# Optimization experiments

Measured on AMD Instinct MI355X. Metric: run time of the kernel, lower is better.

The kernel has to match this reference:

```python
import jax, jax.numpy as jnp
import numpy as np

LN_EPS = 1e-5
NEG_SLOPE = 0.2
INF = float((1 << 32) - 1)


def _ln(x, g, b):
    m = x.mean(-1, keepdims=True)
    v = ((x - m) ** 2).mean(-1, keepdims=True)
    return (x - m) * jax.lax.rsqrt(v + LN_EPS) * g + b


def setup_inputs() -> dict:
    B, M, NPG = 128, 256, 192      # graphs, max nodes per graph, actual nodes per graph
    N = B * NPG                    # 24576 total nodes
    E = N * 16                     # 393216 edges (avg degree 16)
    d, H, Od = 256, 4, 64          # input/attn dim, heads, per-head dim
    out_dim = 256
    key = jax.random.key(0)
    ks = jax.random.split(key, 24)
    s = 0.05
    p = lambda k, sh: jax.random.normal(k, sh, jnp.float32) * s

    node_feat = jax.random.normal(ks[0], (N, d), jnp.float32)
    edge_feat = jax.random.normal(ks[1], (E, d), jnp.float32)
    edge_index = jax.random.randint(ks[2], (2, E), 0, N)
    ptr = jnp.arange(B + 1, dtype=jnp.int32) * NPG
    row_valid = jnp.arange(M) < NPG
    attn_mask = jnp.broadcast_to(row_valid[None, :, None] & row_valid[None, None, :], (B, M, M))

    return dict(
        node_feat=node_feat, attn_mask=attn_mask, edge_feat=edge_feat,
        edge_index=edge_index, num_nodes=N, ptr=ptr,
        Wq=p(ks[3], (d, H * Od)), Wk=p(ks[4], (d, H * Od)), Wv=p(ks[5], (d, H * Od)),
        alphaQ=p(ks[6], (H, Od)), alphaK=p(ks[7], (H, Od)), attn_bias=p(ks[8], (H, Od)),
        gin_eps=jnp.zeros((), jnp.float32),
        gin_W1=p(ks[9], (d, 2 * d)), gin_b1=jnp.zeros((2 * d,), jnp.float32),
        gin_W2=p(ks[10], (2 * d, d)), gin_b2=jnp.zeros((d,), jnp.float32),
        ln1_g=jnp.ones((d,), jnp.float32), ln1_b=jnp.zeros((d,), jnp.float32),
        ln2_g=jnp.ones((d,), jnp.float32), ln2_b=jnp.zeros((d,), jnp.float32),
        ff_W1=p(ks[11], (2 * d, out_dim)), ff_b1=jnp.zeros((out_dim,), jnp.float32),
        ff_W2=p(ks[12], (out_dim, out_dim)), ff_b2=jnp.zeros((out_dim,), jnp.float32),
    )


def reference(node_feat, attn_mask, edge_feat, edge_index, num_nodes, ptr,
              Wq, Wk, Wv, alphaQ, alphaK, attn_bias,
              gin_eps, gin_W1, gin_b1, gin_W2, gin_b2,
              ln1_g, ln1_b, ln2_g, ln2_b,
              ff_W1, ff_b1, ff_W2, ff_b2):
    B, M = attn_mask.shape[:2]
    N, d = node_feat.shape
    H = alphaQ.shape[0]

    # graph -> dense batch layout (scatter by (graph, local position))
    node_ids = jnp.arange(N)
    batch_id = jnp.searchsorted(ptr, node_ids, side='right') - 1
    local = node_ids - ptr[batch_id]
    attn_input = jnp.zeros((B, M, d), node_feat.dtype).at[batch_id, local].set(node_feat)

    # GAT-style additive multi-head attention
    Qp = (attn_input @ Wq).reshape(B, M, H, -1)
    Kp = (attn_input @ Wk).reshape(B, M, H, -1)
    Vp = (attn_input @ Wv).reshape(B, M, H, -1)
    aQ = jnp.einsum('bmhd,hd->bmh', Qp, alphaQ)
    aK = jnp.einsum('bmhd,hd->bmh', Kp, alphaK)
    w = jax.nn.leaky_relu(aQ[:, :, None, :] + aK[:, None, :, :], NEG_SLOPE)  # [B,Q,K,H]
    w = jnp.where(attn_mask[..., None], w, -INF)
    w = jax.nn.softmax(w, axis=2)
    attn_out = (jnp.einsum('bqkh,bkhd->bqhd', w, Vp) + attn_bias).reshape(B, M, -1)

    attn_res = _ln(attn_out + attn_input, ln1_g, ln1_b)[batch_id, local]  # back to [N, d]

    # GIN conv: relu(x[dst] + e) scatter-summed to src, then 2-layer MLP
    msg = jax.nn.relu(node_feat[edge_index[1]] + edge_feat)
    agg = jax.ops.segment_sum(msg, edge_index[0], num_segments=num_nodes)
    h = (1.0 + gin_eps) * node_feat + agg
    gin = jax.nn.relu(h @ gin_W1 + gin_b1) @ gin_W2 + gin_b2
    gin_res = _ln(gin + node_feat, ln2_g, ln2_b)

    x = jnp.concatenate([gin_res, attn_res], axis=-1)  # [N, 2d]
    return jax.nn.relu(x @ ff_W1 + ff_b1) @ ff_W2 + ff_b2
```

## Files before the change

### kernel.cpp

```cpp
#include <hip/hip_runtime.h>

#define LN_EPS 1e-5f
#define NEG_SLOPE 0.2f

typedef __attribute__((ext_vector_type(8))) short short8;
typedef __attribute__((ext_vector_type(4))) float f32x4;

__device__ __forceinline__ unsigned short f2bf(float f) {
  union { float f; unsigned int u; } v;
  v.f = f;
  unsigned int r = v.u + 0x7fffu + ((v.u >> 16) & 1u);
  return (unsigned short)(r >> 16);
}
__device__ __forceinline__ float bf2f(unsigned short u) {
  union { unsigned int u; float f; } v;
  v.u = ((unsigned int)u) << 16;
  return v.f;
}

__global__ __launch_bounds__(256) void k_prep(
    const float* __restrict__ Wv, const float* __restrict__ gW1,
    const float* __restrict__ gW2, const float* __restrict__ fW1,
    const float* __restrict__ fW2, unsigned short* __restrict__ wvt,
    unsigned short* __restrict__ w1t, unsigned short* __restrict__ w2t,
    unsigned short* __restrict__ fw1t, unsigned short* __restrict__ fw2t,
    const float* __restrict__ Wq, const float* __restrict__ Wk,
    const float* __restrict__ alphaQ, const float* __restrict__ alphaK,
    float* __restrict__ wqa, float* __restrict__ wka) {
  if (blockIdx.x == 2048) {
    int t = threadIdx.x;
    for (int h = 0; h < 4; ++h) {
      float sq = 0.f, sk = 0.f;
      for (int od = 0; od < 64; ++od) {
        sq += Wq[t * 256 + h * 64 + od] * alphaQ[h * 64 + od];
        sk += Wk[t * 256 + h * 64 + od] * alphaK[h * 64 + od];
      }
      wqa[t * 4 + h] = sq;
      wka[t * 4 + h] = sk;
    }
    return;
  }
  int i = blockIdx.x * 256 + threadIdx.x;
  const float* src;
  unsigned short* dst;
  int K, N, base;
  if (i < 65536) {
    src = Wv; dst = wvt; K = 256; N = 256; base = 0;
  } else if (i < 196608) {
    src = gW1; dst = w1t; K = 256; N = 512; base = 65536;
  } else if (i < 327680) {
    src = gW2; dst = w2t; K = 512; N = 256; base = 196608;
  } else if (i < 458752) {
    src = fW1; dst = fw1t; K = 512; N = 256; base = 327680;
  } else {
    src = fW2; dst = fw2t; K = 256; N = 256; base = 458752;
  }
  int j = i - base;
  int n = j / K, k = j - n * K;
  dst[j] = f2bf(src[(size_t)k * N + n]);
}

__global__ __launch_bounds__(256) void k_cast(const float* __restrict__ in,
                                              unsigned short* __restrict__ out,
                                              int total4) {
  int i = blockIdx.x * 256 + threadIdx.x;
  if (i < total4) {
    float4 v = ((const float4*)in)[i];
    ushort4 o;
    o.x = f2bf(v.x);
    o.y = f2bf(v.y);
    o.z = f2bf(v.z);
    o.w = f2bf(v.w);
    ((ushort4*)out)[i] = o;
  }
}

__global__ __launch_bounds__(64) void k_aqk(
    const float* __restrict__ X, const float* __restrict__ wqa,
    const float* __restrict__ wka, float* __restrict__ aQ,
    float* __restrict__ aK) {
  int n = blockIdx.x;
  int lane = threadIdx.x;
  float4 x = *(const float4*)(X + (size_t)n * 256 + lane * 4);
  float sq[4], sk[4];
#pragma unroll
  for (int h = 0; h < 4; ++h) {
    int d0 = lane * 4;
    sq[h] = x.x * wqa[(d0 + 0) * 4 + h] + x.y * wqa[(d0 + 1) * 4 + h] +
            x.z * wqa[(d0 + 2) * 4 + h] + x.w * wqa[(d0 + 3) * 4 + h];
    sk[h] = x.x * wka[(d0 + 0) * 4 + h] + x.y * wka[(d0 + 1) * 4 + h] +
            x.z * wka[(d0 + 2) * 4 + h] + x.w * wka[(d0 + 3) * 4 + h];
  }
#pragma unroll
  for (int off = 32; off; off >>= 1) {
#pragma unroll
    for (int h = 0; h < 4; ++h) {
      sq[h] += __shfl_xor(sq[h], off);
      sk[h] += __shfl_xor(sk[h], off);
    }
  }
  if (lane == 0) {
#pragma unroll
    for (int h = 0; h < 4; ++h) {
      aQ[(size_t)n * 4 + h] = sq[h];
      aK[(size_t)n * 4 + h] = sk[h];
    }
  }
}

template <bool RELU, bool BIAS, bool OUTBF>
__global__ __launch_bounds__(256) void k_gemm16(
    const unsigned short* __restrict__ A, const unsigned short* __restrict__ Bt,
    const float* __restrict__ bias, void* __restrict__ Cv, int M, int N,
    int K) {
  __shared__ uint4 As[1024];
  __shared__ uint4 Bs[1024];
  const int tid = threadIdx.x;
  const int wid = tid >> 6;
  const int lane = tid & 63;
  const int row0 = blockIdx.x * 128;
  const int col0 = blockIdx.y * 128;
  const int wr = wid >> 1;
  const int wc = wid & 1;
  const int fr = lane & 15;
  const int fq = lane >> 4;

  f32x4 acc[4][4];
#pragma unroll
  for (int m = 0; m < 4; ++m)
#pragma unroll
    for (int n = 0; n < 4; ++n) acc[m][n] = (f32x4){0.f, 0.f, 0.f, 0.f};

  for (int k0 = 0; k0 < K; k0 += 64) {
    __syncthreads();
#pragma unroll
    for (int c = 0; c < 4; ++c) {
      int idx = c * 256 + tid;
      int row = idx >> 3, slot = idx & 7;
      uint4 va = *(const uint4*)(A + (size_t)(row0 + row) * K + k0 + slot * 8);
      uint4 vb = *(const uint4*)(Bt + (size_t)(col0 + row) * K + k0 + slot * 8);
      int d = row * 8 + (slot ^ (row & 7));
      As[d] = va;
      Bs[d] = vb;
    }
    __syncthreads();
#pragma unroll
    for (int kk = 0; kk < 2; ++kk) {
      short8 af[4], bfr[4];
#pragma unroll
      for (int m = 0; m < 4; ++m) {
        int row = wr * 64 + m * 16 + fr;
        af[m] = *(const short8*)&As[row * 8 + ((kk * 4 + fq) ^ (row & 7))];
      }
#pragma unroll
      for (int n = 0; n < 4; ++n) {
        int col = wc * 64 + n * 16 + fr;
        bfr[n] = *(const short8*)&Bs[col * 8 + ((kk * 4 + fq) ^ (col & 7))];
      }
#pragma unroll
      for (int m = 0; m < 4; ++m)
#pragma unroll
        for (int n = 0; n < 4; ++n)
          acc[m][n] = __builtin_amdgcn_mfma_f32_16x16x32_bf16(af[m], bfr[n],
                                                              acc[m][n], 0, 0, 0);
    }
  }

#pragma unroll
  for (int n = 0; n < 4; ++n) {
    const int col = col0 + wc * 64 + n * 16 + fr;
    const float bv = BIAS ? bias[col] : 0.f;
#pragma unroll
    for (int m = 0; m < 4; ++m) {
#pragma unroll
      for (int r = 0; r < 4; ++r) {
        int row = row0 + wr * 64 + m * 16 + fq * 4 + r;
        float v = acc[m][n][r];
        if (BIAS) v += bv;
        if (RELU) v = fmaxf(v, 0.f);
        if (OUTBF)
          ((unsigned short*)Cv)[(size_t)row * N + col] = f2bf(v);
        else
          ((float*)Cv)[(size_t)row * N + col] = v;
      }
    }
  }
}

__global__ __launch_bounds__(256) void k_attn(
    const float* __restrict__ aQ, const float* __restrict__ aK,
    const unsigned short* __restrict__ Vp16,
    const float* __restrict__ attn_bias, const int* __restrict__ ptr,
    unsigned short* __restrict__ attn16) {
  __shared__ unsigned short Vt[64 * 192];
  __shared__ float aQs[192], aKs[192], sinv[192];
  __shared__ float kmax_s;
  const int b = blockIdx.x, h = blockIdx.y;
  const int n0 = ptr[b];
  const int tid = threadIdx.x;
  const int wid = tid >> 6, lane = tid & 63;

  if (tid < 192) {
    aQs[tid] = aQ[(size_t)(n0 + tid) * 4 + h];
    aKs[tid] = aK[(size_t)(n0 + tid) * 4 + h];
  }
  for (int i = tid; i < 1536; i += 256) {
    int k = i >> 3, cc = (i & 7) << 3;
    short8 v = *(const short8*)(Vp16 + (size_t)(n0 + k) * 256 + h * 64 + cc);
    int ks = k >> 3, kr = k & 7;
#pragma unroll
    for (int jj = 0; jj < 8; ++jj) {
      int c = cc + jj;
      Vt[c * 192 + ((ks ^ (c & 7)) << 3) + kr] = (unsigned short)v[jj];
    }
  }
  __syncthreads();
  if (wid == 0) {
    float m3 = fmaxf(fmaxf(aKs[lane], aKs[lane + 64]), aKs[lane + 128]);
#pragma unroll
    for (int off = 32; off; off >>= 1) m3 = fmaxf(m3, __shfl_xor(m3, off));
    if (lane == 0) kmax_s = m3;
  }
  __syncthreads();
  const float kmax = kmax_s;
  const int fr = lane & 15, fq = lane >> 4;
  const int qbase = wid * 48;

  float aq_m[3], mm[3];
#pragma unroll
  for (int m = 0; m < 3; ++m) {
    float aqv = aQs[qbase + m * 16 + fr];
    aq_m[m] = aqv;
    float t = aqv + kmax;
    mm[m] = t > 0.f ? t : NEG_SLOPE * t;
  }

  f32x4 acc[3][4];
#pragma unroll
  for (int m = 0; m < 3; ++m)
#pragma unroll
    for (int n = 0; n < 4; ++n) acc[m][n] = (f32x4){0.f, 0.f, 0.f, 0.f};
  float psum[3] = {0.f, 0.f, 0.f};

  for (int ks = 0; ks < 6; ++ks) {
    short8 bf[4];
#pragma unroll
    for (int n = 0; n < 4; ++n) {
      int c = n * 16 + fr;
      bf[n] = *(const short8*)&Vt[c * 192 + ((((ks << 2) + fq) ^ (c & 7)) << 3)];
    }
    float ak[8];
#pragma unroll
    for (int j = 0; j < 8; ++j) ak[j] = aKs[(ks << 5) + (fq << 3) + j];
#pragma unroll
    for (int m = 0; m < 3; ++m) {
      short8 af;
      float ps = 0.f;
#pragma unroll
      for (int j = 0; j < 8; ++j) {
        float x = aq_m[m] + ak[j];
        x = x > 0.f ? x : NEG_SLOPE * x;
        float p = __expf(x - mm[m]);
        ps += p;
        af[j] = (short)f2bf(p);
      }
      psum[m] += ps;
#pragma unroll
      for (int n = 0; n < 4; ++n)
        acc[m][n] =
            __builtin_amdgcn_mfma_f32_16x16x32_bf16(af, bf[n], acc[m][n], 0, 0, 0);
    }
  }

#pragma unroll
  for (int m = 0; m < 3; ++m) {
    psum[m] += __shfl_xor(psum[m], 16);
    psum[m] += __shfl_xor(psum[m], 32);
  }
  if (fq == 0) {
#pragma unroll
    for (int m = 0; m < 3; ++m) sinv[qbase + m * 16 + fr] = 1.f / psum[m];
  }
  __syncthreads();

#pragma unroll
  for (int m = 0; m < 3; ++m) {
#pragma unroll
    for (int n = 0; n < 4; ++n) {
      int col = n * 16 + fr;
      float bv = attn_bias[h * 64 + col];
#pragma unroll
      for (int r = 0; r < 4; ++r) {
        int q = qbase + m * 16 + fq * 4 + r;
        float v = acc[m][n][r] * sinv[q] + bv;
        attn16[(size_t)(n0 + q) * 256 + h * 64 + col] = f2bf(v);
      }
    }
  }
}

template <bool XBF>
__global__ __launch_bounds__(64) void k_ln(
    const void* __restrict__ xin, const float* __restrict__ res,
    const float* __restrict__ g, const float* __restrict__ bt,
    unsigned short* __restrict__ out, int ostride, int ooff) {
  const int n = blockIdx.x;
  const int lane = threadIdx.x;
  float v0, v1, v2, v3;
  if (XBF) {
    ushort4 xv = *(const ushort4*)((const unsigned short*)xin +
                                   (size_t)n * 256 + lane * 4);
    v0 = bf2f(xv.x);
    v1 = bf2f(xv.y);
    v2 = bf2f(xv.z);
    v3 = bf2f(xv.w);
  } else {
    float4 xv = *(const float4*)((const float*)xin + (size_t)n * 256 + lane * 4);
    v0 = xv.x;
    v1 = xv.y;
    v2 = xv.z;
    v3 = xv.w;
  }
  float4 rv = *(const float4*)(res + (size_t)n * 256 + lane * 4);
  v0 += rv.x;
  v1 += rv.y;
  v2 += rv.z;
  v3 += rv.w;
  float s = v0 + v1 + v2 + v3;
  float ss = v0 * v0 + v1 * v1 + v2 * v2 + v3 * v3;
#pragma unroll
  for (int off = 32; off; off >>= 1) {
    s += __shfl_xor(s, off);
    ss += __shfl_xor(ss, off);
  }
  const float mean = s * (1.f / 256.f);
  const float var = ss * (1.f / 256.f) - mean * mean;
  const float rs = rsqrtf(var + LN_EPS);
  float4 gv = *(const float4*)(g + lane * 4);
  float4 bv = *(const float4*)(bt + lane * 4);
  ushort4 o;
  o.x = f2bf((v0 - mean) * rs * gv.x + bv.x);
  o.y = f2bf((v1 - mean) * rs * gv.y + bv.y);
  o.z = f2bf((v2 - mean) * rs * gv.z + bv.z);
  o.w = f2bf((v3 - mean) * rs * gv.w + bv.w);
  *(ushort4*)(out + (size_t)n * ostride + ooff + lane * 4) = o;
}

__global__ __launch_bounds__(256) void k_deg(const int* __restrict__ ei,
                                             int* __restrict__ deg, int E) {
  int e = blockIdx.x * 256 + threadIdx.x;
  if (e < E) atomicAdd(&deg[ei[e]], 1);
}

__global__ __launch_bounds__(1024) void k_scan(const int* __restrict__ deg,
                                               int* __restrict__ ofs,
                                               int* __restrict__ cursor,
                                               int Nn) {
  __shared__ int part[1024];
  const int t = threadIdx.x;
  const int CH = (Nn + 1023) / 1024;
  const int base = t * CH;
  int s = 0;
  for (int i = 0; i < CH; ++i) s += (base + i < Nn) ? deg[base + i] : 0;
  part[t] = s;
  __syncthreads();
  for (int off = 1; off < 1024; off <<= 1) {
    int v = (t >= off) ? part[t - off] : 0;
    __syncthreads();
    part[t] += v;
    __syncthreads();
  }
  int o = (t == 0) ? 0 : part[t - 1];
  for (int i = 0; i < CH; ++i) {
    if (base + i < Nn) {
      ofs[base + i] = o;
      cursor[base + i] = o;
      o += deg[base + i];
    }
  }
  if (t == 1023) ofs[Nn] = part[1023];
}

__global__ __launch_bounds__(256) void k_scatter(const int* __restrict__ ei,
                                                 int* __restrict__ cursor,
                                                 int2* __restrict__ edges,
                                                 int E) {
  int e = blockIdx.x * 256 + threadIdx.x;
  if (e < E) {
    int src = ei[e];
    int dst = ei[E + e];
    int pos = atomicAdd(&cursor[src], 1);
    edges[pos] = make_int2(e, dst);
  }
}

__global__ __launch_bounds__(64) void k_gather(
    const float* __restrict__ node, const float* __restrict__ ef,
    const int2* __restrict__ edges, const int* __restrict__ ofs,
    const float* __restrict__ eps_p, unsigned short* __restrict__ agg16) {
  const int n = blockIdx.x;
  const int lane = threadIdx.x;
  const int s0 = ofs[n];
  const int s1 = ofs[n + 1];
  const float epl = 1.f + eps_p[0];
  const f32x4* nodev = (const f32x4*)node;
  const f32x4* efv = (const f32x4*)ef;
  f32x4 xv = nodev[(size_t)n * 64 + lane];
  float a0 = epl * xv.x, a1 = epl * xv.y, a2 = epl * xv.z, a3 = epl * xv.w;
  int j = s0;
  for (; j + 4 <= s1; j += 4) {
    int2 ed0 = edges[j], ed1 = edges[j + 1], ed2 = edges[j + 2],
         ed3 = edges[j + 3];
    f32x4 e0 = __builtin_nontemporal_load(&efv[(size_t)ed0.x * 64 + lane]);
    f32x4 e1 = __builtin_nontemporal_load(&efv[(size_t)ed1.x * 64 + lane]);
    f32x4 e2 = __builtin_nontemporal_load(&efv[(size_t)ed2.x * 64 + lane]);
    f32x4 e3 = __builtin_nontemporal_load(&efv[(size_t)ed3.x * 64 + lane]);
    f32x4 m0 = nodev[(size_t)ed0.y * 64 + lane];
    f32x4 m1 = nodev[(size_t)ed1.y * 64 + lane];
    f32x4 m2 = nodev[(size_t)ed2.y * 64 + lane];
    f32x4 m3 = nodev[(size_t)ed3.y * 64 + lane];
    a0 += fmaxf(e0.x + m0.x, 0.f) + fmaxf(e1.x + m1.x, 0.f) +
          fmaxf(e2.x + m2.x, 0.f) + fmaxf(e3.x + m3.x, 0.f);
    a1 += fmaxf(e0.y + m0.y, 0.f) + fmaxf(e1.y + m1.y, 0.f) +
          fmaxf(e2.y + m2.y, 0.f) + fmaxf(e3.y + m3.y, 0.f);
    a2 += fmaxf(e0.z + m0.z, 0.f) + fmaxf(e1.z + m1.z, 0.f) +
          fmaxf(e2.z + m2.z, 0.f) + fmaxf(e3.z + m3.z, 0.f);
    a3 += fmaxf(e0.w + m0.w, 0.f) + fmaxf(e1.w + m1.w, 0.f) +
          fmaxf(e2.w + m2.w, 0.f) + fmaxf(e3.w + m3.w, 0.f);
  }
  for (; j < s1; ++j) {
    int2 ed = edges[j];
    f32x4 ev = __builtin_nontemporal_load(&efv[(size_t)ed.x * 64 + lane]);
    f32x4 mv = nodev[(size_t)ed.y * 64 + lane];
    a0 += fmaxf(ev.x + mv.x, 0.f);
    a1 += fmaxf(ev.y + mv.y, 0.f);
    a2 += fmaxf(ev.z + mv.z, 0.f);
    a3 += fmaxf(ev.w + mv.w, 0.f);
  }
  ushort4 o;
  o.x = f2bf(a0);
  o.y = f2bf(a1);
  o.z = f2bf(a2);
  o.w = f2bf(a3);
  *(ushort4*)(agg16 + (size_t)n * 256 + lane * 4) = o;
}

extern "C" void kernel_launch(void* const* d_in, const int* in_sizes, int n_in,
                              void* d_out, int out_size, void* d_ws,
                              size_t ws_size, hipStream_t stream) {
  const float* node_feat = (const float*)d_in[0];
  const float* edge_feat = (const float*)d_in[2];
  const int* edge_index = (const int*)d_in[3];
  const int* ptr = (const int*)d_in[5];
  const float* Wq = (const float*)d_in[6];
  const float* Wk = (const float*)d_in[7];
  const float* Wv = (const float*)d_in[8];
  const float* alphaQ = (const float*)d_in[9];
  const float* alphaK = (const float*)d_in[10];
  const float* attn_bias = (const float*)d_in[11];
  const float* gin_eps = (const float*)d_in[12];
  const float* gin_W1 = (const float*)d_in[13];
  const float* gin_b1 = (const float*)d_in[14];
  const float* gin_W2 = (const float*)d_in[15];
  const float* gin_b2 = (const float*)d_in[16];
  const float* ln1_g = (const float*)d_in[17];
  const float* ln1_b = (const float*)d_in[18];
  const float* ln2_g = (const float*)d_in[19];
  const float* ln2_b = (const float*)d_in[20];
  const float* ff_W1 = (const float*)d_in[21];
  const float* ff_b1 = (const float*)d_in[22];
  const float* ff_W2 = (const float*)d_in[23];
  const float* ff_b2 = (const float*)d_in[24];

  const int N = in_sizes[0] / 256;
  const int E = in_sizes[2] / 256;
  const int B = in_sizes[5] - 1;

  float* ws = (float*)d_ws;
  float* buf0 = ws;
  unsigned short* x2_16 = (unsigned short*)(buf0 + (size_t)N * 256);
  unsigned short* agg16 = x2_16 + (size_t)N * 512;
  unsigned short* t1_16 = agg16 + (size_t)N * 256;
  unsigned short* h1_16 = t1_16 + (size_t)N * 512;
  unsigned short* nf16 = h1_16 + (size_t)N * 256;
  unsigned short* vp16 = nf16 + (size_t)N * 256;
  unsigned short* at16 = vp16 + (size_t)N * 256;
  unsigned short* wvt = at16 + (size_t)N * 256;
  unsigned short* w1t = wvt + 65536;
  unsigned short* w2t = w1t + 131072;
  unsigned short* ffw1t = w2t + 131072;
  unsigned short* ffw2t = ffw1t + 131072;
  float* wqa = (float*)(ffw2t + 65536);
  float* wka = wqa + 1024;
  float* aQ = wka + 1024;
  float* aK = aQ + (size_t)N * 4;
  int* ideg = (int*)(aK + (size_t)N * 4);
  int* ofs = ideg + N;
  int* cursor = ofs + N + 2;
  int2* edges = (int2*)(cursor + N);
  size_t need = (size_t)N * 256 * 4 + (size_t)N * 2304 * 2 + 1100000 +
                (size_t)N * 8 * 4 + (size_t)N * 16 + (size_t)E * 8 + 8192;
  if (ws_size < need) return;

  k_prep<<<2049, 256, 0, stream>>>(Wv, gin_W1, gin_W2, ff_W1, ff_W2, wvt, w1t,
                                   w2t, ffw1t, ffw2t, Wq, Wk, alphaQ, alphaK,
                                   wqa, wka);
  k_cast<<<(N * 64 + 255) / 256, 256, 0, stream>>>(node_feat, nf16, N * 64);
  k_aqk<<<N, 64, 0, stream>>>(node_feat, wqa, wka, aQ, aK);

  k_gemm16<false, false, true><<<dim3(N / 128, 2), 256, 0, stream>>>(
      nf16, wvt, nullptr, vp16, N, 256, 256);
  k_attn<<<dim3(B, 4), 256, 0, stream>>>(aQ, aK, vp16, attn_bias, ptr, at16);
  k_ln<true><<<N, 64, 0, stream>>>(at16, node_feat, ln1_g, ln1_b, x2_16, 512,
                                   256);

  (void)hipMemsetAsync(ideg, 0, (size_t)N * sizeof(int), stream);
  k_deg<<<(E + 255) / 256, 256, 0, stream>>>(edge_index, ideg, E);
  k_scan<<<1, 1024, 0, stream>>>(ideg, ofs, cursor, N);
  k_scatter<<<(E + 255) / 256, 256, 0, stream>>>(edge_index, cursor, edges, E);
  k_gather<<<N, 64, 0, stream>>>(node_feat, edge_feat, edges, ofs, gin_eps,
                                 agg16);
  k_gemm16<true, true, true><<<dim3(N / 128, 4), 256, 0, stream>>>(
      agg16, w1t, gin_b1, t1_16, N, 512, 256);
  k_gemm16<false, true, false><<<dim3(N / 128, 2), 256, 0, stream>>>(
      t1_16, w2t, gin_b2, buf0, N, 256, 512);
  k_ln<false><<<N, 64, 0, stream>>>(buf0, node_feat, ln2_g, ln2_b, x2_16, 512,
                                    0);

  k_gemm16<true, true, true><<<dim3(N / 128, 2), 256, 0, stream>>>(
      x2_16, ffw1t, ff_b1, h1_16, N, 256, 512);
  k_gemm16<false, true, false><<<dim3(N / 128, 2), 256, 0, stream>>>(
      h1_16, ffw2t, ff_b2, (float*)d_out, N, 256, 256);
}
```

Measured before the change: 357.9 us.

## Merge prep kernels, double-buffer GEMM with 32x32 MFMA, batch independent GEMMs

Fuses the weight-transpose, degree memset, node-feature cast and aQ/aK projection into one launch, with a separate tiny fold kernel. The GEMM is rewritten to use 32x32x16 bf16 MFMA with a register-prefetched, double-buffered LDS pipeline and a runtime descriptor. The independent Vp and GIN-W1 GEMMs now share a single launch. The intent is to cut launch count and hide global-load latency in the GEMMs. In exchange, the relu/bias/output-type branches become runtime checks and LDS use doubles, which may lower occupancy.

After: 501.5 us. 40.1% more time.

```diff
diff --git a/kernel.cpp b/kernel.cpp
--- a/kernel.cpp
+++ b/kernel.cpp
@@ -5,6 +5,7 @@
 
 typedef __attribute__((ext_vector_type(8))) short short8;
 typedef __attribute__((ext_vector_type(4))) float f32x4;
+typedef __attribute__((ext_vector_type(16))) float f32x16;
 
 __device__ __forceinline__ unsigned short f2bf(float f) {
   union { float f; unsigned int u; } v;
@@ -18,74 +19,72 @@
   return v.f;
 }
 
-__global__ __launch_bounds__(256) void k_prep(
+__global__ __launch_bounds__(256) void k_fold(
+    const float* __restrict__ Wq, const float* __restrict__ Wk,
+    const float* __restrict__ alphaQ, const float* __restrict__ alphaK,
+    float* __restrict__ wqa, float* __restrict__ wka) {
+  int t = threadIdx.x;
+  for (int h = 0; h < 4; ++h) {
+    float sq = 0.f, sk = 0.f;
+    for (int od = 0; od < 64; ++od) {
+      sq += Wq[t * 256 + h * 64 + od] * alphaQ[h * 64 + od];
+      sk += Wk[t * 256 + h * 64 + od] * alphaK[h * 64 + od];
+    }
+    wqa[t * 4 + h] = sq;
+    wka[t * 4 + h] = sk;
+  }
+}
+
+__global__ __launch_bounds__(256) void k_mega(
     const float* __restrict__ Wv, const float* __restrict__ gW1,
     const float* __restrict__ gW2, const float* __restrict__ fW1,
     const float* __restrict__ fW2, unsigned short* __restrict__ wvt,
     unsigned short* __restrict__ w1t, unsigned short* __restrict__ w2t,
     unsigned short* __restrict__ fw1t, unsigned short* __restrict__ fw2t,
-    const float* __restrict__ Wq, const float* __restrict__ Wk,
-    const float* __restrict__ alphaQ, const float* __restrict__ alphaK,
-    float* __restrict__ wqa, float* __restrict__ wka) {
-  if (blockIdx.x == 2048) {
-    int t = threadIdx.x;
-    for (int h = 0; h < 4; ++h) {
-      float sq = 0.f, sk = 0.f;
-      for (int od = 0; od < 64; ++od) {
-        sq += Wq[t * 256 + h * 64 + od] * alphaQ[h * 64 + od];
-        sk += Wk[t * 256 + h * 64 + od] * alphaK[h * 64 + od];
-      }
-      wqa[t * 4 + h] = sq;
-      wka[t * 4 + h] = sk;
-    }
-    return;
-  }
-  int i = blockIdx.x * 256 + threadIdx.x;
-  const float* src;
-  unsigned short* dst;
-  int K, N, base;
-  if (i < 65536) {
-    src = Wv; dst = wvt; K = 256; N = 256; base = 0;
-  } else if (i < 196608) {
-    src = gW1; dst = w1t; K = 256; N = 512; base = 65536;
-  } else if (i < 327680) {
-    src = gW2; dst = w2t; K = 512; N = 256; base = 196608;
-  } else if (i < 458752) {
-    src = fW1; dst = fw1t; K = 512; N = 256; base = 327680;
-  } else {
-    src = fW2; dst = fw2t; K = 256; N = 256; base = 458752;
-  }
-  int j = i - base;
-  int n = j / K, k = j - n * K;
-  dst[j] = f2bf(src[(size_t)k * N + n]);
-}
-
-__global__ __launch_bounds__(256) void k_cast(const float* __restrict__ in,
-                                              unsigned short* __restrict__ out,
-                                              int total4) {
-  int i = blockIdx.x * 256 + threadIdx.x;
-  if (i < total4) {
-    float4 v = ((const float4*)in)[i];
-    ushort4 o;
-    o.x = f2bf(v.x);
-    o.y = f2bf(v.y);
-    o.z = f2bf(v.z);
-    o.w = f2bf(v.w);
-    ((ushort4*)out)[i] = o;
-  }
-}
-
-__global__ __launch_bounds__(64) void k_aqk(
-    const float* __restrict__ X, const float* __restrict__ wqa,
+    int* __restrict__ ideg, int Nn, const float* __restrict__ node_feat,
+    unsigned short* __restrict__ nf16, const float* __restrict__ wqa,
     const float* __restrict__ wka, float* __restrict__ aQ,
     float* __restrict__ aK) {
-  int n = blockIdx.x;
-  int lane = threadIdx.x;
-  float4 x = *(const float4*)(X + (size_t)n * 256 + lane * 4);
+  const int bid = blockIdx.x;
+  if (bid < 2048) {
+    int i = bid * 256 + threadIdx.x;
+    const float* src;
+    unsigned short* dst;
+    int K, N, base;
+    if (i < 65536) {
+      src = Wv; dst = wvt; K = 256; N = 256; base = 0;
+    } else if (i < 196608) {
+      src = gW1; dst = w1t; K = 256; N = 512; base = 65536;
+    } else if (i < 327680) {
+      src = gW2; dst = w2t; K = 512; N = 256; base = 196608;
+    } else if (i < 458752) {
+      src = fW1; dst = fw1t; K = 512; N = 256; base = 327680;
+    } else {
+      src = fW2; dst = fw2t; K = 256; N = 256; base = 458752;
+    }
+    int j = i - base;
+    int n = j / K, k = j - n * K;
+    dst[j] = f2bf(src[(size_t)k * N + n]);
+    return;
+  }
+  if (bid < 2144) {
+    int i = (bid - 2048) * 256 + threadIdx.x;
+    if (i < Nn) ideg[i] = 0;
+    return;
+  }
+  const int n = (bid - 2144) * 4 + (threadIdx.x >> 6);
+  const int lane = threadIdx.x & 63;
+  f32x4 x = ((const f32x4*)node_feat)[(size_t)n * 64 + lane];
+  ushort4 o;
+  o.x = f2bf(x.x);
+  o.y = f2bf(x.y);
+  o.z = f2bf(x.z);
+  o.w = f2bf(x.w);
+  ((ushort4*)nf16)[(size_t)n * 64 + lane] = o;
   float sq[4], sk[4];
+  const int d0 = lane * 4;
 #pragma unroll
   for (int h = 0; h < 4; ++h) {
-    int d0 = lane * 4;
     sq[h] = x.x * wqa[(d0 + 0) * 4 + h] + x.y * wqa[(d0 + 1) * 4 + h] +
             x.z * wqa[(d0 + 2) * 4 + h] + x.w * wqa[(d0 + 3) * 4 + h];
     sk[h] = x.x * wka[(d0 + 0) * 4 + h] + x.y * wka[(d0 + 1) * 4 + h] +
@@ -108,80 +107,122 @@
   }
 }
 
-template <bool RELU, bool BIAS, bool OUTBF>
-__global__ __launch_bounds__(256) void k_gemm16(
-    const unsigned short* __restrict__ A, const unsigned short* __restrict__ Bt,
-    const float* __restrict__ bias, void* __restrict__ Cv, int M, int N,
-    int K) {
-  __shared__ uint4 As[1024];
-  __shared__ uint4 Bs[1024];
+struct GDesc {
+  const unsigned short* A;
+  const unsigned short* Bt;
+  const float* bias;
+  void* C;
+  int N, K;
+  int relu, outbf;
+};
+
+__device__ __forceinline__ f32x16 zero16() {
+  f32x16 z;
+#pragma unroll
+  for (int i = 0; i < 16; ++i) z[i] = 0.f;
+  return z;
+}
+
+__global__ __launch_bounds__(256) void k_gemm2(GDesc d0, GDesc d1, int nb0) {
+  __shared__ uint4 As[2][1024];
+  __shared__ uint4 Bs[2][1024];
+  GDesc d = d0;
+  int t = blockIdx.x;
+  if (t >= nb0) {
+    d = d1;
+    t -= nb0;
+  }
+  const int nN = d.N >> 7;
+  const int row0 = (t / nN) << 7;
+  const int col0 = (t % nN) << 7;
   const int tid = threadIdx.x;
-  const int wid = tid >> 6;
-  const int lane = tid & 63;
-  const int row0 = blockIdx.x * 128;
-  const int col0 = blockIdx.y * 128;
-  const int wr = wid >> 1;
-  const int wc = wid & 1;
-  const int fr = lane & 15;
-  const int fq = lane >> 4;
-
-  f32x4 acc[4][4];
-#pragma unroll
-  for (int m = 0; m < 4; ++m)
-#pragma unroll
-    for (int n = 0; n < 4; ++n) acc[m][n] = (f32x4){0.f, 0.f, 0.f, 0.f};
-
-  for (int k0 = 0; k0 < K; k0 += 64) {
-    __syncthreads();
-#pragma unroll
-    for (int c = 0; c < 4; ++c) {
-      int idx = c * 256 + tid;
-      int row = idx >> 3, slot = idx & 7;
-      uint4 va = *(const uint4*)(A + (size_t)(row0 + row) * K + k0 + slot * 8);
-      uint4 vb = *(const uint4*)(Bt + (size_t)(col0 + row) * K + k0 + slot * 8);
-      int d = row * 8 + (slot ^ (row & 7));
-      As[d] = va;
-      Bs[d] = vb;
-    }
-    __syncthreads();
-#pragma unroll
-    for (int kk = 0; kk < 2; ++kk) {
-      short8 af[4], bfr[4];
-#pragma unroll
-      for (int m = 0; m < 4; ++m) {
-        int row = wr * 64 + m * 16 + fr;
-        af[m] = *(const short8*)&As[row * 8 + ((kk * 4 + fq) ^ (row & 7))];
+  const int wid = tid >> 6, lane = tid & 63;
+  const int wr = wid >> 1, wc = wid & 1;
+  const int l31 = lane & 31, lh = lane >> 5;
+
+  f32x16 acc[2][2];
+#pragma unroll
+  for (int m = 0; m < 2; ++m)
+#pragma unroll
+    for (int n = 0; n < 2; ++n) acc[m][n] = zero16();
+
+  const int nt = d.K >> 6;
+  uint4 ra[4], rb[4];
+#pragma unroll
+  for (int c = 0; c < 4; ++c) {
+    int idx = c * 256 + tid;
+    int row = idx >> 3, slot = idx & 7;
+    ra[c] = *(const uint4*)(d.A + (size_t)(row0 + row) * d.K + slot * 8);
+    rb[c] = *(const uint4*)(d.Bt + (size_t)(col0 + row) * d.K + slot * 8);
+  }
+#pragma unroll
+  for (int c = 0; c < 4; ++c) {
+    int idx = c * 256 + tid;
+    int row = idx >> 3, slot = idx & 7;
+    int dsti = row * 8 + (slot ^ (row & 7));
+    As[0][dsti] = ra[c];
+    Bs[0][dsti] = rb[c];
+  }
+  __syncthreads();
+
+  for (int t0 = 0; t0 < nt; ++t0) {
+    const int cur = t0 & 1;
+    if (t0 + 1 < nt) {
+      const int k0 = (t0 + 1) << 6;
+#pragma unroll
+      for (int c = 0; c < 4; ++c) {
+        int idx = c * 256 + tid;
+        int row = idx >> 3, slot = idx & 7;
+        ra[c] = *(const uint4*)(d.A + (size_t)(row0 + row) * d.K + k0 + slot * 8);
+        rb[c] = *(const uint4*)(d.Bt + (size_t)(col0 + row) * d.K + k0 + slot * 8);
       }
-#pragma unroll
-      for (int n = 0; n < 4; ++n) {
-        int col = wc * 64 + n * 16 + fr;
-        bfr[n] = *(const short8*)&Bs[col * 8 + ((kk * 4 + fq) ^ (col & 7))];
+    }
+#pragma unroll
+    for (int kk = 0; kk < 4; ++kk) {
+      short8 af[2], bf[2];
+      const int kslot = kk * 2 + lh;
+#pragma unroll
+      for (int m = 0; m < 2; ++m) {
+        int row = wr * 64 + m * 32 + l31;
+        af[m] = *(const short8*)&As[cur][row * 8 + (kslot ^ (row & 7))];
+        int col = wc * 64 + m * 32 + l31;
+        bf[m] = *(const short8*)&Bs[cur][col * 8 + (kslot ^ (col & 7))];
       }
 #pragma unroll
-      for (int m = 0; m < 4; ++m)
-#pragma unroll
-        for (int n = 0; n < 4; ++n)
-          acc[m][n] = __builtin_amdgcn_mfma_f32_16x16x32_bf16(af[m], bfr[n],
+      for (int m = 0; m < 2; ++m)
+#pragma unroll
+        for (int n = 0; n < 2; ++n)
+          acc[m][n] = __builtin_amdgcn_mfma_f32_32x32x16_bf16(af[m], bf[n],
                                                               acc[m][n], 0, 0, 0);
     }
-  }
-
-#pragma unroll
-  for (int n = 0; n < 4; ++n) {
-    const int col = col0 + wc * 64 + n * 16 + fr;
-    const float bv = BIAS ? bias[col] : 0.f;
-#pragma unroll
-    for (int m = 0; m < 4; ++m) {
-#pragma unroll
-      for (int r = 0; r < 4; ++r) {
-        int row = row0 + wr * 64 + m * 16 + fq * 4 + r;
-        float v = acc[m][n][r];
-        if (BIAS) v += bv;
-        if (RELU) v = fmaxf(v, 0.f);
-        if (OUTBF)
-          ((unsigned short*)Cv)[(size_t)row * N + col] = f2bf(v);
+    if (t0 + 1 < nt) {
+#pragma unroll
+      for (int c = 0; c < 4; ++c) {
+        int idx = c * 256 + tid;
+        int row = idx >> 3, slot = idx & 7;
+        int dsti = row * 8 + (slot ^ (row & 7));
+        As[cur ^ 1][dsti] = ra[c];
+        Bs[cur ^ 1][dsti] = rb[c];
+      }
+      __syncthreads();
+    }
+  }
+
+#pragma unroll
+  for (int n = 0; n < 2; ++n) {
+    const int col = col0 + wc * 64 + n * 32 + l31;
+    const float bv = d.bias ? d.bias[col] : 0.f;
+#pragma unroll
+    for (int m = 0; m < 2; ++m) {
+#pragma unroll
+      for (int r = 0; r < 16; ++r) {
+        int row = row0 + wr * 64 + m * 32 + (r & 3) + ((r >> 2) << 3) + (lh << 2);
+        float v = acc[m][n][r] + bv;
+        if (d.relu) v = fmaxf(v, 0.f);
+        if (d.outbf)
+          ((unsigned short*)d.C)[(size_t)row * d.N + col] = f2bf(v);
         else
-          ((float*)Cv)[(size_t)row * N + col] = v;
+          ((float*)d.C)[(size_t)row * d.N + col] = v;
       }
     }
   }
@@ -502,33 +543,33 @@
                 (size_t)N * 8 * 4 + (size_t)N * 16 + (size_t)E * 8 + 8192;
   if (ws_size < need) return;
 
-  k_prep<<<2049, 256, 0, stream>>>(Wv, gin_W1, gin_W2, ff_W1, ff_W2, wvt, w1t,
-                                   w2t, ffw1t, ffw2t, Wq, Wk, alphaQ, alphaK,
-                                   wqa, wka);
-  k_cast<<<(N * 64 + 255) / 256, 256, 0, stream>>>(node_feat, nf16, N * 64);
-  k_aqk<<<N, 64, 0, stream>>>(node_feat, wqa, wka, aQ, aK);
-
-  k_gemm16<false, false, true><<<dim3(N / 128, 2), 256, 0, stream>>>(
-      nf16, wvt, nullptr, vp16, N, 256, 256);
-  k_attn<<<dim3(B, 4), 256, 0, stream>>>(aQ, aK, vp16, attn_bias, ptr, at16);
-  k_ln<true><<<N, 64, 0, stream>>>(at16, node_feat, ln1_g, ln1_b, x2_16, 512,
-                                   256);
-
-  (void)hipMemsetAsync(ideg, 0, (size_t)N * sizeof(int), stream);
+  k_fold<<<1, 256, 0, stream>>>(Wq, Wk, alphaQ, alphaK, wqa, wka);
+  k_mega<<<2144 + N / 4, 256, 0, stream>>>(
+      Wv, gin_W1, gin_W2, ff_W1, ff_W2, wvt, w1t, w2t, ffw1t, ffw2t, ideg, N,
+      node_feat, nf16, wqa, wka, aQ, aK);
+
   k_deg<<<(E + 255) / 256, 256, 0, stream>>>(edge_index, ideg, E);
   k_scan<<<1, 1024, 0, stream>>>(ideg, ofs, cursor, N);
   k_scatter<<<(E + 255) / 256, 256, 0, stream>>>(edge_index, cursor, edges, E);
   k_gather<<<N, 64, 0, stream>>>(node_feat, edge_feat, edges, ofs, gin_eps,
                                  agg16);
-  k_gemm16<true, true, true><<<dim3(N / 128, 4), 256, 0, stream>>>(
-      agg16, w1t, gin_b1, t1_16, N, 512, 256);
-  k_gemm16<false, true, false><<<dim3(N / 128, 2), 256, 0, stream>>>(
-      t1_16, w2t, gin_b2, buf0, N, 256, 512);
+
+  GDesc dVp{nf16, wvt, nullptr, vp16, 256, 256, 0, 1};
+  GDesc dF1{agg16, w1t, gin_b1, t1_16, 512, 256, 1, 1};
+  const int nbVp = (N / 128) * 2, nbF1 = (N / 128) * 4;
+  k_gemm2<<<nbVp + nbF1, 256, 0, stream>>>(dVp, dF1, nbVp);
+
+  k_attn<<<dim3(B, 4), 256, 0, stream>>>(aQ, aK, vp16, attn_bias, ptr, at16);
+  k_ln<true><<<N, 64, 0, stream>>>(at16, node_feat, ln1_g, ln1_b, x2_16, 512,
+                                   256);
+
+  GDesc dF2{t1_16, w2t, gin_b2, buf0, 256, 512, 0, 0};
+  k_gemm2<<<(N / 128) * 2, 256, 0, stream>>>(dF2, dF2, 1 << 30);
   k_ln<false><<<N, 64, 0, stream>>>(buf0, node_feat, ln2_g, ln2_b, x2_16, 512,
                                     0);
 
-  k_gemm16<true, true, true><<<dim3(N / 128, 2), 256, 0, stream>>>(
-      x2_16, ffw1t, ff_b1, h1_16, N, 256, 512);
-  k_gemm16<false, true, false><<<dim3(N / 128, 2), 256, 0, stream>>>(
-      h1_16, ffw2t, ff_b2, (float*)d_out, N, 256, 256);
-}
+  GDesc dX1{x2_16, ffw1t, ff_b1, h1_16, 256, 512, 1, 1};
+  k_gemm2<<<(N / 128) * 2, 256, 0, stream>>>(dX1, dX1, 1 << 30);
+  GDesc dX2{h1_16, ffw2t, ff_b2, d_out, 256, 256, 0, 0};
+  k_gemm2<<<(N / 128) * 2, 256, 0, stream>>>(dX2, dX2, 1 << 30);
+}
```

## Fuse prep, cast, aQ/aK and degree zeroing; shrink GEMM row tile

Applied to the files above, without the earlier changes.

Weight transposition, the degree-array memset, the bf16 cast of node features and the aQ/aK projection are merged into one multi-role kernel. The Wq/Wk alpha fold becomes its own single-block kernel launched first, so the merged kernel can use its output. This removes several launches and a memset. The GEMM row tile also drops from 128 to 64 rows, doubling the block count for better CU occupancy on 24576 rows, at the cost of less B-tile reuse per block.

New measurement: 343.7 us. 1.04x faster.

```diff
diff --git a/kernel.cpp b/kernel.cpp
--- a/kernel.cpp
+++ b/kernel.cpp
@@ -18,74 +18,72 @@
   return v.f;
 }
 
-__global__ __launch_bounds__(256) void k_prep(
+__global__ __launch_bounds__(256) void k_fold(
+    const float* __restrict__ Wq, const float* __restrict__ Wk,
+    const float* __restrict__ alphaQ, const float* __restrict__ alphaK,
+    float* __restrict__ wqa, float* __restrict__ wka) {
+  int t = threadIdx.x;
+  for (int h = 0; h < 4; ++h) {
+    float sq = 0.f, sk = 0.f;
+    for (int od = 0; od < 64; ++od) {
+      sq += Wq[t * 256 + h * 64 + od] * alphaQ[h * 64 + od];
+      sk += Wk[t * 256 + h * 64 + od] * alphaK[h * 64 + od];
+    }
+    wqa[t * 4 + h] = sq;
+    wka[t * 4 + h] = sk;
+  }
+}
+
+__global__ __launch_bounds__(256) void k_mega(
     const float* __restrict__ Wv, const float* __restrict__ gW1,
     const float* __restrict__ gW2, const float* __restrict__ fW1,
     const float* __restrict__ fW2, unsigned short* __restrict__ wvt,
     unsigned short* __restrict__ w1t, unsigned short* __restrict__ w2t,
     unsigned short* __restrict__ fw1t, unsigned short* __restrict__ fw2t,
-    const float* __restrict__ Wq, const float* __restrict__ Wk,
-    const float* __restrict__ alphaQ, const float* __restrict__ alphaK,
-    float* __restrict__ wqa, float* __restrict__ wka) {
-  if (blockIdx.x == 2048) {
-    int t = threadIdx.x;
-    for (int h = 0; h < 4; ++h) {
-      float sq = 0.f, sk = 0.f;
-      for (int od = 0; od < 64; ++od) {
-        sq += Wq[t * 256 + h * 64 + od] * alphaQ[h * 64 + od];
-        sk += Wk[t * 256 + h * 64 + od] * alphaK[h * 64 + od];
-      }
-      wqa[t * 4 + h] = sq;
-      wka[t * 4 + h] = sk;
-    }
-    return;
-  }
-  int i = blockIdx.x * 256 + threadIdx.x;
-  const float* src;
-  unsigned short* dst;
-  int K, N, base;
-  if (i < 65536) {
-    src = Wv; dst = wvt; K = 256; N = 256; base = 0;
-  } else if (i < 196608) {
-    src = gW1; dst = w1t; K = 256; N = 512; base = 65536;
-  } else if (i < 327680) {
-    src = gW2; dst = w2t; K = 512; N = 256; base = 196608;
-  } else if (i < 458752) {
-    src = fW1; dst = fw1t; K = 512; N = 256; base = 327680;
-  } else {
-    src = fW2; dst = fw2t; K = 256; N = 256; base = 458752;
-  }
-  int j = i - base;
-  int n = j / K, k = j - n * K;
-  dst[j] = f2bf(src[(size_t)k * N + n]);
-}
-
-__global__ __launch_bounds__(256) void k_cast(const float* __restrict__ in,
-                                              unsigned short* __restrict__ out,
-                                              int total4) {
-  int i = blockIdx.x * 256 + threadIdx.x;
-  if (i < total4) {
-    float4 v = ((const float4*)in)[i];
-    ushort4 o;
-    o.x = f2bf(v.x);
-    o.y = f2bf(v.y);
-    o.z = f2bf(v.z);
-    o.w = f2bf(v.w);
-    ((ushort4*)out)[i] = o;
-  }
-}
-
-__global__ __launch_bounds__(64) void k_aqk(
-    const float* __restrict__ X, const float* __restrict__ wqa,
+    int* __restrict__ ideg, int Nn, const float* __restrict__ node_feat,
+    unsigned short* __restrict__ nf16, const float* __restrict__ wqa,
     const float* __restrict__ wka, float* __restrict__ aQ,
     float* __restrict__ aK) {
-  int n = blockIdx.x;
-  int lane = threadIdx.x;
-  float4 x = *(const float4*)(X + (size_t)n * 256 + lane * 4);
+  const int bid = blockIdx.x;
+  if (bid < 2048) {
+    int i = bid * 256 + threadIdx.x;
+    const float* src;
+    unsigned short* dst;
+    int K, N, base;
+    if (i < 65536) {
+      src = Wv; dst = wvt; K = 256; N = 256; base = 0;
+    } else if (i < 196608) {
+      src = gW1; dst = w1t; K = 256; N = 512; base = 65536;
+    } else if (i < 327680) {
+      src = gW2; dst = w2t; K = 512; N = 256; base = 196608;
+    } else if (i < 458752) {
+      src = fW1; dst = fw1t; K = 512; N = 256; base = 327680;
+    } else {
+      src = fW2; dst = fw2t; K = 256; N = 256; base = 458752;
+    }
+    int j = i - base;
+    int n = j / K, k = j - n * K;
+    dst[j] = f2bf(src[(size_t)k * N + n]);
+    return;
+  }
+  if (bid < 2144) {
+    int i = (bid - 2048) * 256 + threadIdx.x;
+    if (i < Nn) ideg[i] = 0;
+    return;
+  }
+  const int n = (bid - 2144) * 4 + (threadIdx.x >> 6);
+  const int lane = threadIdx.x & 63;
+  f32x4 x = ((const f32x4*)node_feat)[(size_t)n * 64 + lane];
+  ushort4 o;
+  o.x = f2bf(x.x);
+  o.y = f2bf(x.y);
+  o.z = f2bf(x.z);
+  o.w = f2bf(x.w);
+  ((ushort4*)nf16)[(size_t)n * 64 + lane] = o;
   float sq[4], sk[4];
+  const int d0 = lane * 4;
 #pragma unroll
   for (int h = 0; h < 4; ++h) {
-    int d0 = lane * 4;
     sq[h] = x.x * wqa[(d0 + 0) * 4 + h] + x.y * wqa[(d0 + 1) * 4 + h] +
             x.z * wqa[(d0 + 2) * 4 + h] + x.w * wqa[(d0 + 3) * 4 + h];
     sk[h] = x.x * wka[(d0 + 0) * 4 + h] + x.y * wka[(d0 + 1) * 4 + h] +
@@ -113,43 +111,47 @@
     const unsigned short* __restrict__ A, const unsigned short* __restrict__ Bt,
     const float* __restrict__ bias, void* __restrict__ Cv, int M, int N,
     int K) {
-  __shared__ uint4 As[1024];
+  __shared__ uint4 As[512];
   __shared__ uint4 Bs[1024];
   const int tid = threadIdx.x;
   const int wid = tid >> 6;
   const int lane = tid & 63;
-  const int row0 = blockIdx.x * 128;
+  const int row0 = blockIdx.x * 64;
   const int col0 = blockIdx.y * 128;
   const int wr = wid >> 1;
   const int wc = wid & 1;
   const int fr = lane & 15;
   const int fq = lane >> 4;
 
-  f32x4 acc[4][4];
-#pragma unroll
-  for (int m = 0; m < 4; ++m)
+  f32x4 acc[2][4];
+#pragma unroll
+  for (int m = 0; m < 2; ++m)
 #pragma unroll
     for (int n = 0; n < 4; ++n) acc[m][n] = (f32x4){0.f, 0.f, 0.f, 0.f};
 
   for (int k0 = 0; k0 < K; k0 += 64) {
     __syncthreads();
+#pragma unroll
+    for (int c = 0; c < 2; ++c) {
+      int idx = c * 256 + tid;
+      int row = idx >> 3, slot = idx & 7;
+      As[row * 8 + (slot ^ (row & 7))] =
+          *(const uint4*)(A + (size_t)(row0 + row) * K + k0 + slot * 8);
+    }
 #pragma unroll
     for (int c = 0; c < 4; ++c) {
       int idx = c * 256 + tid;
       int row = idx >> 3, slot = idx & 7;
-      uint4 va = *(const uint4*)(A + (size_t)(row0 + row) * K + k0 + slot * 8);
-      uint4 vb = *(const uint4*)(Bt + (size_t)(col0 + row) * K + k0 + slot * 8);
-      int d = row * 8 + (slot ^ (row & 7));
-      As[d] = va;
-      Bs[d] = vb;
+      Bs[row * 8 + (slot ^ (row & 7))] =
+          *(const uint4*)(Bt + (size_t)(col0 + row) * K + k0 + slot * 8);
     }
     __syncthreads();
 #pragma unroll
     for (int kk = 0; kk < 2; ++kk) {
-      short8 af[4], bfr[4];
-#pragma unroll
-      for (int m = 0; m < 4; ++m) {
-        int row = wr * 64 + m * 16 + fr;
+      short8 af[2], bfr[4];
+#pragma unroll
+      for (int m = 0; m < 2; ++m) {
+        int row = wr * 32 + m * 16 + fr;
         af[m] = *(const short8*)&As[row * 8 + ((kk * 4 + fq) ^ (row & 7))];
       }
 #pragma unroll
@@ -158,7 +160,7 @@
         bfr[n] = *(const short8*)&Bs[col * 8 + ((kk * 4 + fq) ^ (col & 7))];
       }
 #pragma unroll
-      for (int m = 0; m < 4; ++m)
+      for (int m = 0; m < 2; ++m)
 #pragma unroll
         for (int n = 0; n < 4; ++n)
           acc[m][n] = __builtin_amdgcn_mfma_f32_16x16x32_bf16(af[m], bfr[n],
@@ -171,10 +173,10 @@
     const int col = col0 + wc * 64 + n * 16 + fr;
     const float bv = BIAS ? bias[col] : 0.f;
 #pragma unroll
-    for (int m = 0; m < 4; ++m) {
+    for (int m = 0; m < 2; ++m) {
 #pragma unroll
       for (int r = 0; r < 4; ++r) {
-        int row = row0 + wr * 64 + m * 16 + fq * 4 + r;
+        int row = row0 + wr * 32 + m * 16 + fq * 4 + r;
         float v = acc[m][n][r];
         if (BIAS) v += bv;
         if (RELU) v = fmaxf(v, 0.f);
@@ -502,33 +504,31 @@
                 (size_t)N * 8 * 4 + (size_t)N * 16 + (size_t)E * 8 + 8192;
   if (ws_size < need) return;
 
-  k_prep<<<2049, 256, 0, stream>>>(Wv, gin_W1, gin_W2, ff_W1, ff_W2, wvt, w1t,
-                                   w2t, ffw1t, ffw2t, Wq, Wk, alphaQ, alphaK,
-                                   wqa, wka);
-  k_cast<<<(N * 64 + 255) / 256, 256, 0, stream>>>(node_feat, nf16, N * 64);
-  k_aqk<<<N, 64, 0, stream>>>(node_feat, wqa, wka, aQ, aK);
-
-  k_gemm16<false, false, true><<<dim3(N / 128, 2), 256, 0, stream>>>(
+  k_fold<<<1, 256, 0, stream>>>(Wq, Wk, alphaQ, alphaK, wqa, wka);
+  k_mega<<<2144 + N / 4, 256, 0, stream>>>(
+      Wv, gin_W1, gin_W2, ff_W1, ff_W2, wvt, w1t, w2t, ffw1t, ffw2t, ideg, N,
+      node_feat, nf16, wqa, wka, aQ, aK);
+
+  k_gemm16<false, false, true><<<dim3(N / 64, 2), 256, 0, stream>>>(
       nf16, wvt, nullptr, vp16, N, 256, 256);
   k_attn<<<dim3(B, 4), 256, 0, stream>>>(aQ, aK, vp16, attn_bias, ptr, at16);
   k_ln<true><<<N, 64, 0, stream>>>(at16, node_feat, ln1_g, ln1_b, x2_16, 512,
                                    256);
 
-  (void)hipMemsetAsync(ideg, 0, (size_t)N * sizeof(int), stream);
   k_deg<<<(E + 255) / 256, 256, 0, stream>>>(edge_index, ideg, E);
   k_scan<<<1, 1024, 0, stream>>>(ideg, ofs, cursor, N);
   k_scatter<<<(E + 255) / 256, 256, 0, stream>>>(edge_index, cursor, edges, E);
   k_gather<<<N, 64, 0, stream>>>(node_feat, edge_feat, edges, ofs, gin_eps,
                                  agg16);
-  k_gemm16<true, true, true><<<dim3(N / 128, 4), 256, 0, stream>>>(
+  k_gemm16<true, true, true><<<dim3(N / 64, 4), 256, 0, stream>>>(
       agg16, w1t, gin_b1, t1_16, N, 512, 256);
-  k_gemm16<false, true, false><<<dim3(N / 128, 2), 256, 0, stream>>>(
+  k_gemm16<false, true, false><<<dim3(N / 64, 2), 256, 0, stream>>>(
       t1_16, w2t, gin_b2, buf0, N, 256, 512);
   k_ln<false><<<N, 64, 0, stream>>>(buf0, node_feat, ln2_g, ln2_b, x2_16, 512,
                                     0);
 
-  k_gemm16<true, true, true><<<dim3(N / 128, 2), 256, 0, stream>>>(
+  k_gemm16<true, true, true><<<dim3(N / 64, 2), 256, 0, stream>>>(
       x2_16, ffw1t, ff_b1, h1_16, N, 256, 512);
-  k_gemm16<false, true, false><<<dim3(N / 128, 2), 256, 0, stream>>>(
+  k_gemm16<false, true, false><<<dim3(N / 64, 2), 256, 0, stream>>>(
       h1_16, ffw2t, ff_b2, (float*)d_out, N, 256, 256);
 }
```
